# Kernel optimization log

Hardware: AMD Instinct MI355X
Metric: run time of the kernel (lower is better)

The kernel has to match this reference:

```python
import jax, jax.numpy as jnp
import numpy as np

FILTERS = 64
NBITS = 4
NUE = 4
NSPU = 2
NST = NUE * NSPU           # 8 streams total
OUT_CH = NST * NBITS       # 32 output channels
NBS, NANT = 1, 16
CIN = NBS * NANT * 2 + NBS * NANT * NUE * NSPU * 2 + NUE * NSPU + 1  # 297


def hard_sigmoid(x):
    # Keras ConvLSTM2D default recurrent_activation
    return jnp.clip(0.2 * x + 0.5, 0.0, 1.0)


def conv2d(x, w):
    # x: [N,H,W,C], w: [kh,kw,Cin,Cout], SAME padding
    return jax.lax.conv_general_dilated(x, w, (1, 1), 'SAME',
                                        dimension_numbers=('NHWC', 'HWIO', 'NHWC'))


def convlstm2d(x, Wx, Wh, b):
    """Keras ConvLSTM2D (return_sequences=True), gate order i,f,c,o.
    x: [B,T,H,W,Cin] -> [B,T,H,W,F].
    Input-to-hidden convs are precomputed for all timesteps at once;
    only the cheap hidden-to-hidden conv is inside the scan."""
    B, T, H, W, Cin = x.shape
    F = Wh.shape[2]
    xz = conv2d(x.reshape(B * T, H, W, Cin), Wx).reshape(B, T, H, W, 4 * F) + b
    xz = jnp.moveaxis(xz, 1, 0)  # [T,B,H,W,4F]
    h0 = jnp.zeros((B, H, W, F), x.dtype)

    def step(carry, z_in):
        h, c = carry
        z = z_in + conv2d(h, Wh)
        zi, zf, zg, zo = jnp.split(z, 4, axis=-1)
        i = hard_sigmoid(zi)
        f = hard_sigmoid(zf)
        g = jnp.tanh(zg)
        o = hard_sigmoid(zo)
        c = f * c + i * g
        h = o * jnp.tanh(c)
        return (h, c), h

    _, hs = jax.lax.scan(step, (h0, h0), xz)
    return jnp.moveaxis(hs, 0, 1)  # [B,T,H,W,F]


def _lstm_params(key, cin, f, scale=0.05):
    k1, k2, k3 = jax.random.split(key, 3)
    Wx = jax.random.normal(k1, (3, 3, cin, 4 * f), jnp.float32) * scale
    Wh = jax.random.normal(k2, (3, 3, f, 4 * f), jnp.float32) * scale
    b = jax.random.normal(k3, (4 * f,), jnp.float32) * scale
    return Wx, Wh, b


def setup_inputs() -> dict:
    key = jax.random.key(0)
    ks = jax.random.split(key, 10)
    B, T, W = 2, 14, 1536
    inp = {
        'y_ri': jax.random.normal(ks[0], (B, NBS, NANT, T, W, 2), jnp.float32),
        'h_ri': jax.random.normal(ks[1], (B, NBS, NANT, NUE, NSPU, T, W, 2), jnp.float32),
        'err_var': jax.random.uniform(ks[2], (1, 1, 1, NUE, NSPU, T, W), jnp.float32),
        'no': jax.random.uniform(ks[3], (1,), jnp.float32),
    }
    inp['Wx_in'], inp['Wh_in'], inp['b_in'] = _lstm_params(ks[4], CIN, FILTERS)
    inp['Wx_r0'], inp['Wh_r0'], inp['b_r0'] = _lstm_params(ks[5], FILTERS, FILTERS)
    inp['Wx_r1'], inp['Wh_r1'], inp['b_r1'] = _lstm_params(ks[6], FILTERS, FILTERS)
    inp['Wx_out'], inp['Wh_out'], inp['b_out'] = _lstm_params(ks[7], FILTERS, OUT_CH)
    return inp


def _forward(y_ri, h_ri, err_var, no,
             Wx_in, Wh_in, b_in,
             Wx_r0, Wh_r0, b_r0,
             Wx_r1, Wh_r1, b_r1,
             Wx_out, Wh_out, b_out):
    B, nbs, nant, T, W, _ = y_ri.shape
    # y: [B,nbs,nant,T,W,2] -> [B,T,W,nbs*nant*2]
    y_feats = jnp.transpose(y_ri, (0, 3, 4, 1, 2, 5)).reshape(B, T, W, -1)
    # h: [B,nbs,nant,ue,spu,T,W,2] -> [B,T,W,nbs*nant*ue*spu*2]
    h_feats = jnp.transpose(h_ri, (0, 5, 6, 1, 2, 3, 4, 7)).reshape(B, T, W, -1)
    # err_var: [1,1,1,ue,spu,T,W] -> [B,T,W,ue*spu]
    ev = jnp.transpose(err_var[0, 0, 0], (2, 3, 0, 1)).reshape(1, T, W, NUE * NSPU)
    err_feats = jnp.broadcast_to(ev, (B, T, W, NUE * NSPU))
    no_feat = jnp.broadcast_to(no.reshape(1, 1, 1, 1), (B, T, W, 1))
    z = jnp.concatenate([y_feats, h_feats, err_feats, no_feat], axis=-1)
    z = z[:, :, :, None, :]  # [B,T,W,1,C]

    z = convlstm2d(z, Wx_in, Wh_in, b_in)
    # residual blocks (in_ch == filters, so identity skip)
    z = convlstm2d(z, Wx_r0, Wh_r0, b_r0) + z
    z = convlstm2d(z, Wx_r1, Wh_r1, b_r1) + z
    z = convlstm2d(z, Wx_out, Wh_out, b_out)

    z = z[:, :, :, 0, :]  # [B,T,W,OUT_CH]
    N = T * W
    z = z.reshape(B, N, NUE, NSPU, NBITS)
    z = jnp.transpose(z, (0, 2, 3, 1, 4))
    return z.reshape(B, NUE, NSPU, N * NBITS)


def reference(y_ri, h_ri, err_var, no,
              Wx_in, Wh_in, b_in,
              Wx_r0, Wh_r0, b_r0,
              Wx_r1, Wh_r1, b_r1,
              Wx_out, Wh_out, b_out):
    return _forward(y_ri, h_ri, err_var, no,
                    Wx_in, Wh_in, b_in,
                    Wx_r0, Wh_r0, b_r0,
                    Wx_r1, Wh_r1, b_r1,
                    Wx_out, Wh_out, b_out)
```

## Files before the change

kernel.cpp:

```cpp
#include <hip/hip_runtime.h>
#include <hip/hip_bf16.h>


#define BB   2
#define TT   14
#define LL   1536
#define LL2  1538
#define CINR 297
#define CP_IN 320
#define NSTRIP 96
#define NBLK  (BB * NSTRIP)
#define WIN  48

typedef __attribute__((ext_vector_type(8))) short short8;
typedef __attribute__((ext_vector_type(4))) float floatx4;

static constexpr size_t U_WBIN_HI  = 0;
static constexpr size_t U_WBIN_LO  = 245760;
static constexpr size_t U_WBR0_HI  = 491520;
static constexpr size_t U_WBR0_LO  = 540672;
static constexpr size_t U_WBR1_HI  = 589824;
static constexpr size_t U_WBR1_LO  = 638976;
static constexpr size_t U_WBOUT_HI = 688128;
static constexpr size_t U_WBOUT_LO = 712704;
static constexpr size_t U_WHTIN    = 737280;
static constexpr size_t U_WHTR0    = 786432;
static constexpr size_t U_WHTR1    = 835584;
static constexpr size_t U_WHTOUT   = 884736;
static constexpr size_t OFF_BIN   = 448512;
static constexpr size_t OFF_BR0   = 448768;
static constexpr size_t OFF_BR1   = 449024;
static constexpr size_t OFF_BOUT  = 449280;
static constexpr size_t OFF_Z0HI  = 458752;
static constexpr size_t SZ_Z0PL   = 6890240;
static constexpr size_t OFF_Z0LO  = OFF_Z0HI + SZ_Z0PL;
static constexpr size_t OFF_XZ    = OFF_Z0LO + SZ_Z0PL;
static constexpr size_t SZ_XZ     = (size_t)BB*TT*LL*256;
static constexpr size_t OFF_SEQ   = OFF_Z0HI;
static constexpr size_t OFF_SEQHI = OFF_SEQ + (size_t)BB*TT*LL2*64;
static constexpr size_t OFF_SEQLO = OFF_SEQHI + (size_t)BB*TT*LL2*32;

__device__ __forceinline__ float hsig(float x) {
    return fminf(fmaxf(0.2f * x + 0.5f, 0.0f), 1.0f);
}
__device__ __forceinline__ float ftanh(float x) {
    float e = __expf(2.0f * x);
    return 1.0f - 2.0f / (e + 1.0f);
}
__device__ __forceinline__ unsigned short f2bf(float x) {
    unsigned int u = __builtin_bit_cast(unsigned int, x);
    u += 0x7fffu + ((u >> 16) & 1u);
    return (unsigned short)(u >> 16);
}
__device__ __forceinline__ float bf2f(unsigned short h) {
    unsigned int u = ((unsigned int)h) << 16;
    return __builtin_bit_cast(float, u);
}

__global__ __launch_bounds__(256)
void zero_pads_kernel(unsigned short* __restrict__ z0hi,
                      unsigned short* __restrict__ z0lo)
{
    int idx = blockIdx.x * 256 + threadIdx.x;
    const int NZ = BB * TT * 2 * CP_IN;
    if (idx < NZ) {
        int c = idx % CP_IN, r2 = idx / CP_IN;
        int p = r2 >> 1, e = r2 & 1;
        long long off = ((long long)p * LL2 + (e ? (LL2 - 1) : 0)) * CP_IN + c;
        z0hi[off] = 0; z0lo[off] = 0;
    }
}

__global__ __launch_bounds__(256)
void zero_seq_pads_kernel(unsigned short* __restrict__ seqhb,
                          unsigned short* __restrict__ seqlb)
{
    int idx = blockIdx.x * 256 + threadIdx.x;
    const int NS = BB * TT * 2 * 64;
    if (idx < NS) {
        int c = idx % 64, r2 = idx / 64;
        int p = r2 >> 1, e = r2 & 1;
        long long off = ((long long)p * LL2 + (e ? (LL2 - 1) : 0)) * 64 + c;
        seqhb[off] = 0; seqlb[off] = 0;
    }
}

__global__ __launch_bounds__(256)
void prep_weights_kernel(const float* wx_in, const float* wh_in, const float* b_in,
                         const float* wx_r0, const float* wh_r0, const float* b_r0,
                         const float* wx_r1, const float* wh_r1, const float* b_r1,
                         const float* wx_out, const float* wh_out, const float* b_out,
                         float* __restrict__ ws)
{
    int idx = blockIdx.x * 256 + threadIdx.x;
    unsigned short* u = (unsigned short*)ws;
    if (idx < 245760) {
        int j = idx & 7, lane = (idx >> 3) & 63, frag = idx >> 9;
        int g = frag & 15, rest = frag >> 4;
        int kh = rest % 3, cc = rest / 3;
        int mm = lane & 15, quad = lane >> 4;
        int n = g * 16 + mm;
        int ci = cc * 32 + quad * 8 + j;
        float v = 0.0f;
        if (ci < CINR)
            v = wx_in[((size_t)(kh * 3 + 1) * CINR + ci) * 256 + (n & 3) * 64 + (n >> 2)];
        unsigned short hi = f2bf(v);
        u[U_WBIN_HI + idx] = hi;
        u[U_WBIN_LO + idx] = f2bf(v - bf2f(hi));
        return;
    }
    idx -= 245760;
    if (idx < 49152) {
        int j = idx & 7, lane = (idx >> 3) & 63, frag = idx >> 9;
        int g = frag & 15, rest = frag >> 4;
        int kh = rest % 3, cc = rest / 3;
        int mm = lane & 15, quad = lane >> 4;
        int n = g * 16 + mm;
        int ci = cc * 32 + quad * 8 + j;
        float v = wx_r0[((size_t)(kh * 3 + 1) * 64 + ci) * 256 + (n & 3) * 64 + (n >> 2)];
        unsigned short hi = f2bf(v);
        u[U_WBR0_HI + idx] = hi;
        u[U_WBR0_LO + idx] = f2bf(v - bf2f(hi));
        return;
    }
    idx -= 49152;
    if (idx < 49152) {
        int j = idx & 7, lane = (idx >> 3) & 63, frag = idx >> 9;
        int g = frag & 15, rest = frag >> 4;
        int kh = rest % 3, cc = rest / 3;
        int mm = lane & 15, quad = lane >> 4;
        int n = g * 16 + mm;
        int ci = cc * 32 + quad * 8 + j;
        float v = wx_r1[((size_t)(kh * 3 + 1) * 64 + ci) * 256 + (n & 3) * 64 + (n >> 2)];
        unsigned short hi = f2bf(v);
        u[U_WBR1_HI + idx] = hi;
        u[U_WBR1_LO + idx] = f2bf(v - bf2f(hi));
        return;
    }
    idx -= 49152;
    if (idx < 24576) {
        int j = idx & 7, lane = (idx >> 3) & 63, frag = idx >> 9;
        int g = frag & 7, rest = frag >> 3;
        int kh = rest % 3, cc = rest / 3;
        int mm = lane & 15, quad = lane >> 4;
        int n = g * 16 + mm;
        int ci = cc * 32 + quad * 8 + j;
        float v = wx_out[((size_t)(kh * 3 + 1) * 64 + ci) * 128 + (n & 3) * 32 + (n >> 2)];
        unsigned short hi = f2bf(v);
        u[U_WBOUT_HI + idx] = hi;
        u[U_WBOUT_LO + idx] = f2bf(v - bf2f(hi));
        return;
    }
    idx -= 24576;
    if (idx < 49152) {
        int n = idx / 192, k = idx % 192, kh = k >> 6, ci = k & 63;
        u[U_WHTIN + idx] = f2bf(wh_in[((size_t)(kh * 3 + 1) * 64 + ci) * 256 + n]);
        return;
    }
    idx -= 49152;
    if (idx < 49152) {
        int n = idx / 192, k = idx % 192, kh = k >> 6, ci = k & 63;
        u[U_WHTR0 + idx] = f2bf(wh_r0[((size_t)(kh * 3 + 1) * 64 + ci) * 256 + n]);
        return;
    }
    idx -= 49152;
    if (idx < 49152) {
        int n = idx / 192, k = idx % 192, kh = k >> 6, ci = k & 63;
        u[U_WHTR1 + idx] = f2bf(wh_r1[((size_t)(kh * 3 + 1) * 64 + ci) * 256 + n]);
        return;
    }
    idx -= 49152;
    if (idx < 12288) {
        int n = idx / 96, k = idx % 96, kh = k / 32, ci = k % 32;
        u[U_WHTOUT + idx] = f2bf(wh_out[((size_t)(kh * 3 + 1) * 32 + ci) * 128 + n]);
        return;
    }
    idx -= 12288;
    if (idx < 256) { int f = idx >> 2, g = idx & 3; ws[OFF_BIN + idx] = b_in[g * 64 + f]; return; }
    idx -= 256;
    if (idx < 256) { int f = idx >> 2, g = idx & 3; ws[OFF_BR0 + idx] = b_r0[g * 64 + f]; return; }
    idx -= 256;
    if (idx < 256) { int f = idx >> 2, g = idx & 3; ws[OFF_BR1 + idx] = b_r1[g * 64 + f]; return; }
    idx -= 256;
    if (idx < 128) { int f = idx >> 2, g = idx & 3; ws[OFF_BOUT + idx] = b_out[g * 32 + f]; return; }
}

__global__ __launch_bounds__(256)
void build_features_kernel(const float* __restrict__ y,
                           const float* __restrict__ h,
                           const float* __restrict__ ev,
                           const float* __restrict__ no,
                           unsigned short* __restrict__ z0hi,
                           unsigned short* __restrict__ z0lo)
{
    long long idx = (long long)blockIdx.x * 256 + threadIdx.x;
    const long long total = (long long)BB * TT * LL * CP_IN;
    if (idx >= total) return;
    int c = (int)(idx % CP_IN);
    long long rest = idx / CP_IN;
    int l = (int)(rest % LL); rest /= LL;
    int t = (int)(rest % TT);
    int b = (int)(rest / TT);
    float v = 0.0f;
    if (c < 32) {
        int na = c >> 1, ri = c & 1;
        v = y[((((long long)b * 16 + na) * TT + t) * LL + l) * 2 + ri];
    } else if (c < 288) {
        int q = c - 32;
        int ri = q & 1, nspu = (q >> 1) & 1, nue = (q >> 2) & 3, na = q >> 4;
        v = h[((((((long long)b * 16 + na) * 4 + nue) * 2 + nspu) * TT + t) * LL + l) * 2 + ri];
    } else if (c < 296) {
        int q = c - 288; int nspu = q & 1, nue = q >> 1;
        v = ev[(((long long)(nue * 2 + nspu) * TT + t) * LL) + l];
    } else if (c == 296) {
        v = no[0];
    }
    const long long widx = (((long long)(b * TT + t)) * LL2 + (l + 1)) * CP_IN + c;
    unsigned short hi = f2bf(v);
    z0hi[widx] = hi;
    z0lo[widx] = f2bf(v - bf2f(hi));
}

template <int CP>
__global__ __launch_bounds__(256)
void xz_gemm_mfma_kernel(const unsigned short* __restrict__ Ahi,
                         const unsigned short* __restrict__ Alo,
                         const unsigned short* __restrict__ Bphi,
                         const unsigned short* __restrict__ Bplo,
                         const float* __restrict__ bias,
                         float* __restrict__ out, int Ncol)
{
    constexpr int NCm = CP / 64;
    __shared__ unsigned short AsHi[66 * 72], AsLo[66 * 72];
    const int tid  = threadIdx.x;
    const int lane = tid & 63;
    const int wv   = tid >> 6;
    const int m    = lane & 15;
    const int quad = lane >> 4;
    const int bt   = blockIdx.y;
    const int l0   = blockIdx.x * 64;
    const int n0   = blockIdx.z * 128;
    const int NG   = Ncol >> 4;
    const int gBase = (n0 >> 4) + wv;

    const int r0s = tid >> 3,        c0 = (tid & 7) * 8;
    const int r1s = (tid + 256) >> 3, c1 = (tid & 7) * 8;
    const int r2s = 64 + (tid >> 3),  c2 = (tid & 7) * 8;
    const long long aG0 = ((long long)bt * LL2 + l0 + r0s) * CP + c0;
    const long long aG1 = ((long long)bt * LL2 + l0 + r1s) * CP + c1;
    const long long aG2 = ((long long)bt * LL2 + l0 + r2s) * CP + c2;

    short8 g0h, g0l, g1h, g1l, g2h = (short8)0, g2l = (short8)0;

    g0h = *reinterpret_cast<const short8*>(&Ahi[aG0]);
    g0l = *reinterpret_cast<const short8*>(&Alo[aG0]);
    g1h = *reinterpret_cast<const short8*>(&Ahi[aG1]);
    g1l = *reinterpret_cast<const short8*>(&Alo[aG1]);
    if (tid < 16) {
        g2h = *reinterpret_cast<const short8*>(&Ahi[aG2]);
        g2l = *reinterpret_cast<const short8*>(&Alo[aG2]);
    }

    floatx4 acc[4][2];
#pragma unroll
    for (int i = 0; i < 4; i++)
#pragma unroll
        for (int j = 0; j < 2; j++) acc[i][j] = (floatx4){0.f, 0.f, 0.f, 0.f};

#pragma unroll 1
    for (int mc = 0; mc < NCm; ++mc) {
        __syncthreads();
        *reinterpret_cast<short8*>(&AsHi[r0s * 72 + c0]) = g0h;
        *reinterpret_cast<short8*>(&AsLo[r0s * 72 + c0]) = g0l;
        *reinterpret_cast<short8*>(&AsHi[r1s * 72 + c1]) = g1h;
        *reinterpret_cast<short8*>(&AsLo[r1s * 72 + c1]) = g1l;
        if (tid < 16) {
            *reinterpret_cast<short8*>(&AsHi[r2s * 72 + c2]) = g2h;
            *reinterpret_cast<short8*>(&AsLo[r2s * 72 + c2]) = g2l;
        }
        __syncthreads();
        if (mc + 1 < NCm) {
            const int co = (mc + 1) * 64;
            g0h = *reinterpret_cast<const short8*>(&Ahi[aG0 + co]);
            g0l = *reinterpret_cast<const short8*>(&Alo[aG0 + co]);
            g1h = *reinterpret_cast<const short8*>(&Ahi[aG1 + co]);
            g1l = *reinterpret_cast<const short8*>(&Alo[aG1 + co]);
            if (tid < 16) {
                g2h = *reinterpret_cast<const short8*>(&Ahi[aG2 + co]);
                g2l = *reinterpret_cast<const short8*>(&Alo[aG2 + co]);
            }
        }
#pragma unroll
        for (int sub = 0; sub < 2; ++sub) {
            const int cc = mc * 2 + sub;
            short8 bh[3][2], bl[3][2];
#pragma unroll
            for (int kh = 0; kh < 3; ++kh)
#pragma unroll
                for (int nt = 0; nt < 2; ++nt) {
                    const size_t off =
                        ((size_t)((cc * 3 + kh) * NG + gBase + nt * 4)) * 512 + lane * 8;
                    bh[kh][nt] = *reinterpret_cast<const short8*>(&Bphi[off]);
                    bl[kh][nt] = *reinterpret_cast<const short8*>(&Bplo[off]);
                }
#pragma unroll
            for (int kh = 0; kh < 3; ++kh) {
#pragma unroll
                for (int mt = 0; mt < 4; ++mt) {
                    const int aofs = (mt * 16 + m + kh) * 72 + sub * 32 + quad * 8;
                    const short8 ah = *reinterpret_cast<const short8*>(&AsHi[aofs]);
                    const short8 al = *reinterpret_cast<const short8*>(&AsLo[aofs]);
                    acc[mt][0] = __builtin_amdgcn_mfma_f32_16x16x32_bf16(al, bh[kh][0], acc[mt][0], 0, 0, 0);
                    acc[mt][0] = __builtin_amdgcn_mfma_f32_16x16x32_bf16(ah, bl[kh][0], acc[mt][0], 0, 0, 0);
                    acc[mt][0] = __builtin_amdgcn_mfma_f32_16x16x32_bf16(ah, bh[kh][0], acc[mt][0], 0, 0, 0);
                    acc[mt][1] = __builtin_amdgcn_mfma_f32_16x16x32_bf16(al, bh[kh][1], acc[mt][1], 0, 0, 0);
                    acc[mt][1] = __builtin_amdgcn_mfma_f32_16x16x32_bf16(ah, bl[kh][1], acc[mt][1], 0, 0, 0);
                    acc[mt][1] = __builtin_amdgcn_mfma_f32_16x16x32_bf16(ah, bh[kh][1], acc[mt][1], 0, 0, 0);
                }
            }
        }
    }

#pragma unroll
    for (int nt = 0; nt < 2; ++nt) {
        const int col = n0 + nt * 64 + wv * 16 + m;
        const float bv = bias[col];
#pragma unroll
        for (int mt = 0; mt < 4; ++mt) {
#pragma unroll
            for (int reg = 0; reg < 4; ++reg) {
                int l = l0 + mt * 16 + quad * 4 + reg;
                out[((size_t)bt * LL + l) * Ncol + col] = acc[mt][nt][reg] + bv;
            }
        }
    }
}

template <int F_, bool RESID, bool OUTW>
__global__ __launch_bounds__(64 * (F_ / 16))
void lstm_scan_kernel(const float* __restrict__ xz,
                      const unsigned short* __restrict__ WhT,
                      float* seq,
                      unsigned short* __restrict__ seqhb,
                      unsigned short* __restrict__ seqlb,
                      float* __restrict__ dout)
{
    constexpr int NW = F_ / 16;
    constexpr int NT = 64 * NW;
    constexpr int K  = 3 * F_;
    constexpr int KS = K / 32;
    constexpr int KH = KS / 3;
    constexpr int HP = F_ + 8;
    __shared__ unsigned short Hs[2][(WIN + 2) * HP];

    const int tid  = threadIdx.x;
    const int lane = tid & 63;
    const int wv   = tid >> 6;
    const int m    = lane & 15;
    const int quad = lane >> 4;
    const int blk  = (blockIdx.x & 7) * (NBLK / 8) + (blockIdx.x >> 3);
    const int b    = blk / NSTRIP;
    const int o0   = (blk % NSTRIP) * 16;
    const int f    = wv * 16 + m;

    short8 bfr[4][KS];
#pragma unroll
    for (int g = 0; g < 4; g++)
#pragma unroll
        for (int ks = 0; ks < KS; ks++) {
            const int n  = g * F_ + f;
            const int k0 = ks * 32 + quad * 8;
            bfr[g][ks] = *reinterpret_cast<const short8*>(&WhT[(size_t)n * K + k0]);
        }

    for (int idx = tid; idx < (WIN + 2) * HP; idx += NT) {
        Hs[0][idx] = 0; Hs[1][idx] = 0;
    }
    __syncthreads();

    float c[3][4];
#pragma unroll
    for (int i = 0; i < 3; i++)
#pragma unroll
        for (int j = 0; j < 4; j++) c[i][j] = 0.0f;

    int cur = 0;
    for (int t = 0; t < TT; ++t) {
        const size_t btL  = ((size_t)b * TT + t) * LL;
        const size_t btLP = ((size_t)b * TT + t) * LL2;

        float4 xzv[3][4];
        float  rsv[4];
#pragma unroll
        for (int mt = 0; mt < 3; ++mt)
#pragma unroll
            for (int reg = 0; reg < 4; ++reg) {
                const int w = mt * 16 + quad * 4 + reg;
                const int l = o0 - 16 + w;
                float4 v = make_float4(0.f, 0.f, 0.f, 0.f);
                if (l >= 0 && l < LL && w >= t && w < WIN - t)
                    v = *reinterpret_cast<const float4*>(
                        &xz[(btL + l) * (size_t)(4 * F_) + f * 4]);
                xzv[mt][reg] = v;
            }
        if (RESID) {
#pragma unroll
            for (int reg = 0; reg < 4; ++reg) {
                const int l = o0 + quad * 4 + reg;
                rsv[reg] = seq[(btLP + 1 + l) * F_ + f];
            }
        }

        const int nxt = cur ^ 1;
#pragma unroll
        for (int mt = 0; mt < 3; ++mt) {
            floatx4 zi = {0.f, 0.f, 0.f, 0.f};
            floatx4 zf = {0.f, 0.f, 0.f, 0.f};
            floatx4 zg = {0.f, 0.f, 0.f, 0.f};
            floatx4 zo = {0.f, 0.f, 0.f, 0.f};
            if (t > 0) {
#pragma unroll
                for (int kh = 0; kh < 3; kh++) {
#pragma unroll
                    for (int hf = 0; hf < KH; hf++) {
                        const short8 af = *reinterpret_cast<const short8*>(
                            &Hs[cur][(mt * 16 + m + kh) * HP + hf * 32 + quad * 8]);
                        const int ks = kh * KH + hf;
                        zi = __builtin_amdgcn_mfma_f32_16x16x32_bf16(af, bfr[0][ks], zi, 0, 0, 0);
                        zf = __builtin_amdgcn_mfma_f32_16x16x32_bf16(af, bfr[1][ks], zf, 0, 0, 0);
                        zg = __builtin_amdgcn_mfma_f32_16x16x32_bf16(af, bfr[2][ks], zg, 0, 0, 0);
                        zo = __builtin_amdgcn_mfma_f32_16x16x32_bf16(af, bfr[3][ks], zo, 0, 0, 0);
                    }
                }
            }
#pragma unroll
            for (int reg = 0; reg < 4; ++reg) {
                const int w = mt * 16 + quad * 4 + reg;
                const int l = o0 - 16 + w;
                const bool valid = (l >= 0 && l < LL);
                const float4 z4 = xzv[mt][reg];
                const float ig = hsig(z4.x + zi[reg]);
                const float fg = hsig(z4.y + zf[reg]);
                const float gg = ftanh(z4.z + zg[reg]);
                const float og = hsig(z4.w + zo[reg]);
                float cn = fg * c[mt][reg] + ig * gg;
                float hn = og * ftanh(cn);
                if (!valid) { cn = 0.0f; hn = 0.0f; }
                c[mt][reg] = cn;
                Hs[nxt][(1 + w) * HP + f] = f2bf(hn);
                if (w >= 16 && w < 32) {
                    if (OUTW) {
                        const int ue = f >> 3, spu = (f >> 2) & 1, bit = f & 3;
                        const size_t n = (size_t)t * LL + l;
                        dout[(((size_t)b * 4 + ue) * 2 + spu) * ((size_t)TT * LL * 4)
                             + n * 4 + bit] = hn;
                    } else {
                        float v = hn;
                        if (RESID) v += rsv[reg];
                        seq[(btLP + 1 + l) * F_ + f] = v;
                        const unsigned short hi2 = f2bf(v);
                        seqhb[(btLP + 1 + l) * F_ + f] = hi2;
                        seqlb[(btLP + 1 + l) * F_ + f] = f2bf(v - bf2f(hi2));
                    }
                }
            }
        }
        __syncthreads();
        cur = nxt;
    }
}

extern "C" void kernel_launch(void* const* d_in, const int* in_sizes, int n_in,
                              void* d_out, int out_size, void* d_ws, size_t ws_size,
                              hipStream_t stream)
{
    (void)in_sizes; (void)n_in; (void)out_size; (void)ws_size;
    const float* y_ri   = (const float*)d_in[0];
    const float* h_ri   = (const float*)d_in[1];
    const float* evar   = (const float*)d_in[2];
    const float* no     = (const float*)d_in[3];
    const float* wx_in  = (const float*)d_in[4];
    const float* wh_in  = (const float*)d_in[5];
    const float* b_in   = (const float*)d_in[6];
    const float* wx_r0  = (const float*)d_in[7];
    const float* wh_r0  = (const float*)d_in[8];
    const float* b_r0   = (const float*)d_in[9];
    const float* wx_r1  = (const float*)d_in[10];
    const float* wh_r1  = (const float*)d_in[11];
    const float* b_r1   = (const float*)d_in[12];
    const float* wx_out = (const float*)d_in[13];
    const float* wh_out = (const float*)d_in[14];
    const float* b_out  = (const float*)d_in[15];

    float* ws = (float*)d_ws;
    unsigned short* wu = (unsigned short*)d_ws;
    float* dout = (float*)d_out;

    unsigned short* z0hi = (unsigned short*)(ws + OFF_Z0HI);
    unsigned short* z0lo = (unsigned short*)(ws + OFF_Z0LO);
    float* xz    = ws + OFF_XZ;
    float* seq   = ws + OFF_SEQ;
    unsigned short* seqhb = (unsigned short*)(ws + OFF_SEQHI);
    unsigned short* seqlb = (unsigned short*)(ws + OFF_SEQLO);

    zero_pads_kernel<<<70, 256, 0, stream>>>(z0hi, z0lo);
    prep_weights_kernel<<<2068, 256, 0, stream>>>(
        wx_in, wh_in, b_in, wx_r0, wh_r0, b_r0,
        wx_r1, wh_r1, b_r1, wx_out, wh_out, b_out, ws);
    {
        long long total = (long long)BB * TT * LL * CP_IN;
        int blocks = (int)((total + 255) / 256);
        build_features_kernel<<<blocks, 256, 0, stream>>>(
            y_ri, h_ri, evar, no, z0hi, z0lo);
    }

    const dim3 gIn(LL / 64, BB * TT, 2);
    const dim3 gO (LL / 64, BB * TT, 1);

    xz_gemm_mfma_kernel<CP_IN><<<gIn, 256, 0, stream>>>(
        z0hi, z0lo, wu + U_WBIN_HI, wu + U_WBIN_LO, ws + OFF_BIN, xz, 256);
    zero_seq_pads_kernel<<<14, 256, 0, stream>>>(seqhb, seqlb);
    lstm_scan_kernel<64, false, false><<<NBLK, 256, 0, stream>>>(
        xz, wu + U_WHTIN, seq, seqhb, seqlb, nullptr);

    xz_gemm_mfma_kernel<64><<<gIn, 256, 0, stream>>>(
        seqhb, seqlb, wu + U_WBR0_HI, wu + U_WBR0_LO, ws + OFF_BR0, xz, 256);
    lstm_scan_kernel<64, true, false><<<NBLK, 256, 0, stream>>>(
        xz, wu + U_WHTR0, seq, seqhb, seqlb, nullptr);

    xz_gemm_mfma_kernel<64><<<gIn, 256, 0, stream>>>(
        seqhb, seqlb, wu + U_WBR1_HI, wu + U_WBR1_LO, ws + OFF_BR1, xz, 256);
    lstm_scan_kernel<64, true, false><<<NBLK, 256, 0, stream>>>(
        xz, wu + U_WHTR1, seq, seqhb, seqlb, nullptr);

    xz_gemm_mfma_kernel<64><<<gO, 256, 0, stream>>>(
        seqhb, seqlb, wu + U_WBOUT_HI, wu + U_WBOUT_LO, ws + OFF_BOUT, xz, 128);
    lstm_scan_kernel<32, false, true><<<NBLK, 128, 0, stream>>>(
        xz, wu + U_WHTOUT, nullptr, nullptr, nullptr, dout);
}
```

Baseline: 486.2 us.

## Prefetch next timestep's input gates into LDS via async global_load_lds

Replaces the per-timestep register loads of the precomputed input-gate tensor with a double-buffered LDS staging area filled by direct global-to-LDS loads for timestep t+1 while timestep t is computed. The aim is to hide global memory latency behind the recurrent MFMA work in the scan loop. It costs extra LDS (two full windows of 4F floats per row), which can lower occupancy. It also drops the triangular w>=t skipping, so every step loads the full window.

```diff
diff --git a/kernel.cpp b/kernel.cpp
--- a/kernel.cpp
+++ b/kernel.cpp
@@ -56,6 +56,11 @@
     unsigned int u = ((unsigned int)h) << 16;
     return __builtin_bit_cast(float, u);
 }
+__device__ __forceinline__ void gload_lds16(const void* g, void* l) {
+    __builtin_amdgcn_global_load_lds(
+        (const __attribute__((address_space(1))) unsigned int*)g,
+        (__attribute__((address_space(3))) unsigned int*)l, 16, 0, 0);
+}
 
 __global__ __launch_bounds__(256)
 void zero_pads_kernel(unsigned short* __restrict__ z0hi,
@@ -351,7 +356,12 @@
     constexpr int KS = K / 32;
     constexpr int KH = KS / 3;
     constexpr int HP = F_ + 8;
+    constexpr int ROWF = 4 * F_;
+    constexpr int NCHK = WIN * ROWF / 256;
+    constexpr int CPW  = NCHK / NW;
+    constexpr int RPC  = 256 / ROWF;
     __shared__ unsigned short Hs[2][(WIN + 2) * HP];
+    __shared__ float Xs[2][WIN * ROWF];
 
     const int tid  = threadIdx.x;
     const int lane = tid & 63;
@@ -376,6 +386,19 @@
     for (int idx = tid; idx < (WIN + 2) * HP; idx += NT) {
         Hs[0][idx] = 0; Hs[1][idx] = 0;
     }
+    for (int idx = tid; idx < 2 * WIN * ROWF; idx += NT)
+        (&Xs[0][0])[idx] = 0.0f;
+    __syncthreads();
+
+#pragma unroll
+    for (int kk = 0; kk < CPW; ++kk) {
+        const int k = wv * CPW + kk;
+        const int l0c = o0 - 16 + k * RPC;
+        if (l0c >= 0 && l0c + RPC <= LL) {
+            const float* gp = xz + ((long long)b * TT * LL + l0c) * ROWF + lane * 4;
+            gload_lds16(gp, &Xs[0][k * 256]);
+        }
+    }
     __syncthreads();
 
     float c[3][4];
@@ -389,20 +412,7 @@
         const size_t btL  = ((size_t)b * TT + t) * LL;
         const size_t btLP = ((size_t)b * TT + t) * LL2;
 
-        float4 xzv[3][4];
-        float  rsv[4];
-#pragma unroll
-        for (int mt = 0; mt < 3; ++mt)
-#pragma unroll
-            for (int reg = 0; reg < 4; ++reg) {
-                const int w = mt * 16 + quad * 4 + reg;
-                const int l = o0 - 16 + w;
-                float4 v = make_float4(0.f, 0.f, 0.f, 0.f);
-                if (l >= 0 && l < LL && w >= t && w < WIN - t)
-                    v = *reinterpret_cast<const float4*>(
-                        &xz[(btL + l) * (size_t)(4 * F_) + f * 4]);
-                xzv[mt][reg] = v;
-            }
+        float rsv[4];
         if (RESID) {
 #pragma unroll
             for (int reg = 0; reg < 4; ++reg) {
@@ -412,6 +422,19 @@
         }
 
         const int nxt = cur ^ 1;
+        if (t + 1 < TT) {
+#pragma unroll
+            for (int kk = 0; kk < CPW; ++kk) {
+                const int k = wv * CPW + kk;
+                const int l0c = o0 - 16 + k * RPC;
+                if (l0c >= 0 && l0c + RPC <= LL) {
+                    const float* gp = xz + (((long long)b * TT + t + 1) * LL + l0c) * ROWF
+                                    + lane * 4;
+                    gload_lds16(gp, &Xs[nxt][k * 256]);
+                }
+            }
+        }
+
 #pragma unroll
         for (int mt = 0; mt < 3; ++mt) {
             floatx4 zi = {0.f, 0.f, 0.f, 0.f};
@@ -438,7 +461,8 @@
                 const int w = mt * 16 + quad * 4 + reg;
                 const int l = o0 - 16 + w;
                 const bool valid = (l >= 0 && l < LL);
-                const float4 z4 = xzv[mt][reg];
+                const float4 z4 = *reinterpret_cast<const float4*>(
+                    &Xs[cur][w * ROWF + f * 4]);
                 const float ig = hsig(z4.x + zi[reg]);
                 const float fg = hsig(z4.y + zf[reg]);
                 const float gg = ftanh(z4.z + zg[reg]);
```

Result: slower. 499.3 us (+2.7%).
